# Kernel optimization log

Hardware: AMD Instinct MI355X
Metric: run time of the kernel (lower is better)

The kernel has to match this reference:

```python
import jax, jax.numpy as jnp
import numpy as np

B, S, D, H = 2, 2048, 1024, 16
DK = D // H

def setup_inputs() -> dict:
    key = jax.random.key(0)
    ks = jax.random.split(key, 9)
    def lin(k, fan_in):
        bound = 1.0 / np.sqrt(fan_in)
        kw, kb = jax.random.split(k)
        w = jax.random.uniform(kw, (D, D), jnp.float32, -bound, bound)
        b = jax.random.uniform(kb, (D,), jnp.float32, -bound, bound)
        return w, b
    Wq_w, Wq_b = lin(ks[0], D)
    Wk_w, Wk_b = lin(ks[1], D)
    Wv_w, Wv_b = lin(ks[2], D)
    Wo_w, Wo_b = lin(ks[3], D)
    x = jax.random.normal(ks[4], (B, S, D), jnp.float32)
    mask = jnp.ones((B, 1, 1, S), jnp.int32)
    return {"x": x, "mask": mask,
            "Wq_w": Wq_w, "Wq_b": Wq_b, "Wk_w": Wk_w, "Wk_b": Wk_b,
            "Wv_w": Wv_w, "Wv_b": Wv_b, "Wo_w": Wo_w, "Wo_b": Wo_b}

def reference(x, mask, Wq_w, Wq_b, Wk_w, Wk_b, Wv_w, Wv_b, Wo_w, Wo_b):
    b, s, d = x.shape
    def split_heads(t):  # [B,S,D] -> [B,H,S,DK]
        return t.reshape(b, s, H, DK).transpose(0, 2, 1, 3)
    Q = split_heads(x @ Wq_w.T + Wq_b)
    K = split_heads(x @ Wk_w.T + Wk_b)
    V = split_heads(x @ Wv_w.T + Wv_b)
    scale = 1.0 / jnp.sqrt(jnp.float32(DK))
    scores = jnp.einsum('bhqd,bhkd->bhqk', Q, K) * scale  # [B,H,S,S]
    scores = jnp.where(mask == 0, jnp.float32(-1e9), scores)
    attn = jax.nn.softmax(scores, axis=-1)
    context = jnp.einsum('bhqk,bhkd->bhqd', attn, V)  # [B,H,S,DK]
    context = context.transpose(0, 2, 1, 3).reshape(b, s, d)
    return context @ Wo_w.T + Wo_b
```

## Files before the change

kernel.cpp:

```cpp
#include <hip/hip_runtime.h>
#include <hip/hip_bf16.h>


#define DEV __device__ __forceinline__

typedef __bf16 bf16_t;
typedef __bf16 bf16x8 __attribute__((ext_vector_type(8)));
typedef float f32x4 __attribute__((ext_vector_type(4)));

constexpr int Ss = 2048, Dd = 1024, Hh = 16, DKk = 64;

DEV void gload_lds16(const void* g, void* l) {
  __builtin_amdgcn_global_load_lds(
      (__attribute__((address_space(1))) void*)(g),
      (__attribute__((address_space(3))) void*)(l), 16, 0, 0);
}

DEV bf16_t f2b(float v) { return (bf16_t)v; }

DEV void cvt16_core(const float* src, bf16_t* dst) {
  const float4* s4 = (const float4*)src;
  float4 a = s4[0], b = s4[1], c = s4[2], d = s4[3];
  bf16x8 lo = {f2b(a.x), f2b(a.y), f2b(a.z), f2b(a.w), f2b(b.x), f2b(b.y), f2b(b.z), f2b(b.w)};
  bf16x8 hi = {f2b(c.x), f2b(c.y), f2b(c.z), f2b(c.w), f2b(d.x), f2b(d.y), f2b(d.z), f2b(d.w)};
  *(bf16x8*)dst = lo;
  *(bf16x8*)(dst + 8) = hi;
}

__global__ __launch_bounds__(256) void cvt16(const float* __restrict__ x,
                                             bf16_t* __restrict__ xb) {
  size_t i = ((size_t)blockIdx.x * 256 + threadIdx.x) * 16;
  cvt16_core(x + i, xb + i);
}

__global__ __launch_bounds__(256) void cvt_w4(
    const float* __restrict__ s0, const float* __restrict__ s1,
    const float* __restrict__ s2, const float* __restrict__ s3,
    bf16_t* __restrict__ dst) {
  int z = blockIdx.y;
  const float* s = (z == 0) ? s0 : ((z == 1) ? s1 : ((z == 2) ? s2 : s3));
  size_t i = ((size_t)blockIdx.x * 256 + threadIdx.x) * 16;
  cvt16_core(s + i, dst + (size_t)z * (1u << 20) + i);
}

template <bool WB16>
__global__ __launch_bounds__(256) void gemm_qkv(
    const bf16_t* __restrict__ A,
    const float* __restrict__ W0, const float* __restrict__ W1, const float* __restrict__ W2,
    const bf16_t* __restrict__ Wb,
    const float* __restrict__ b0, const float* __restrict__ b1, const float* __restrict__ b2,
    bf16_t* __restrict__ o0, bf16_t* __restrict__ o1, bf16_t* __restrict__ o2) {
  const int z = blockIdx.z;
  const float* Wf = (z == 0) ? W0 : ((z == 1) ? W1 : W2);
  const bf16_t* Wbf = Wb + (size_t)z * (1u << 20);
  const float* bias = (z == 0) ? b0 : ((z == 1) ? b1 : b2);
  bf16_t* out = (z == 0) ? o0 : ((z == 1) ? o1 : o2);

  __shared__ __align__(16) bf16_t As[128 * 32];
  __shared__ __align__(16) bf16_t Ws[128 * 32];

  const int tid = threadIdx.x;
  const int lane = tid & 63, w = tid >> 6;
  const int quad = lane >> 4, c = lane & 15;
  const int wm = w >> 1, wn = w & 1;
  const int m0 = blockIdx.y * 128, n0 = blockIdx.x * 128;
  const int trow = tid >> 1, tcol = (tid & 1) * 16;
  const int srow = lane >> 2, scol = (lane & 3) * 8;

  const f32x4 vzero = {0.f, 0.f, 0.f, 0.f};
  f32x4 acc[4][4];
  for (int i = 0; i < 4; i++)
    for (int j = 0; j < 4; j++) acc[i][j] = vzero;

  for (int k0 = 0; k0 < 1024; k0 += 32) {
    for (int r = 0; r < 2; r++) {
      int row = r * 64 + w * 16;
      gload_lds16(&A[(size_t)(m0 + row + srow) * 1024 + k0 + scol], &As[row * 32]);
      if (WB16)
        gload_lds16(&Wbf[(size_t)(n0 + row + srow) * 1024 + k0 + scol], &Ws[row * 32]);
    }
    if (!WB16)
      cvt16_core(&Wf[(size_t)(n0 + trow) * 1024 + k0 + tcol], &Ws[trow * 32 + tcol]);
    __syncthreads();

    bf16x8 af[4], bfr[4];
    for (int i = 0; i < 4; i++)
      af[i] = *(const bf16x8*)&As[(wm * 64 + i * 16 + c) * 32 + quad * 8];
    for (int j = 0; j < 4; j++)
      bfr[j] = *(const bf16x8*)&Ws[(wn * 64 + j * 16 + c) * 32 + quad * 8];
    for (int i = 0; i < 4; i++)
      for (int j = 0; j < 4; j++)
        acc[i][j] = __builtin_amdgcn_mfma_f32_16x16x32_bf16(af[i], bfr[j], acc[i][j], 0, 0, 0);
    __syncthreads();
  }

  for (int j = 0; j < 4; j++) {
    int n = n0 + wn * 64 + j * 16 + c;
    float bv = bias[n];
    for (int i = 0; i < 4; i++) {
      int mbase = m0 + wm * 64 + i * 16 + quad * 4;
      for (int r = 0; r < 4; r++) {
        int m = mbase + r;
        float v = acc[i][j][r] + bv;
        int b_ = m >> 11, s_ = m & 2047, h_ = n >> 6, dk_ = n & 63;
        if (z < 2)
          out[((size_t)(b_ * Hh + h_) * Ss + s_) * DKk + dk_] = f2b(v);
        else
          out[((size_t)(b_ * Hh + h_) * DKk + dk_) * Ss + s_] = f2b(v);
      }
    }
  }
}

__global__ __launch_bounds__(256) void attn_fwd(
    const bf16_t* __restrict__ Q, const bf16_t* __restrict__ K,
    const bf16_t* __restrict__ Vt, const int* __restrict__ mask,
    bf16_t* __restrict__ ctx) {
  __shared__ __align__(16) bf16_t Ks[64 * 64];
  __shared__ __align__(16) bf16_t Vts[64 * 64];
  __shared__ __align__(16) bf16_t Ps[4][16 * 72];

  const int tid = threadIdx.x, lane = tid & 63, w = tid >> 6;
  const int quad = lane >> 4, c = lane & 15;
  const int bh = blockIdx.y, b_ = bh >> 4, h_ = bh & 15;
  const int q0 = blockIdx.x * 64 + w * 16;
  const size_t head = (size_t)bh * Ss * DKk;

  bf16x8 qf[2];
  for (int ks = 0; ks < 2; ks++)
    qf[ks] = *(const bf16x8*)&Q[head + (size_t)(q0 + c) * DKk + ks * 32 + quad * 8];

  const bf16_t oneb = f2b(1.0f);
  const bf16x8 ones = {oneb, oneb, oneb, oneb, oneb, oneb, oneb, oneb};

  const f32x4 vzero = {0.f, 0.f, 0.f, 0.f};
  f32x4 o[4];
  for (int j = 0; j < 4; j++) o[j] = vzero;
  f32x4 ol = vzero;

  const int sr = lane >> 3;
  const int gc = (lane & 7) ^ sr;
  const int c7 = c & 7;

  for (int kt = 0; kt < Ss / 64; kt++) {
    __syncthreads();
    for (int r = 0; r < 2; r++) {
      int row = r * 32 + w * 8;
      gload_lds16(&K[head + (size_t)(kt * 64 + row + sr) * 64 + gc * 8], &Ks[row * 64]);
      gload_lds16(&Vt[head + (size_t)(row + sr) * Ss + kt * 64 + gc * 8], &Vts[row * 64]);
    }
    __syncthreads();

    f32x4 sc[4];
    for (int ni = 0; ni < 4; ni++) sc[ni] = vzero;
    for (int ks = 0; ks < 2; ks++) {
      int pc = ((ks * 4 + quad) ^ c7) * 8;
      for (int ni = 0; ni < 4; ni++) {
        bf16x8 kf = *(const bf16x8*)&Ks[(ni * 16 + c) * 64 + pc];
        sc[ni] = __builtin_amdgcn_mfma_f32_16x16x32_bf16(qf[ks], kf, sc[ni], 0, 0, 0);
      }
    }

    for (int ni = 0; ni < 4; ni++) {
      int mk = mask[b_ * Ss + kt * 64 + ni * 16 + c];
      for (int r = 0; r < 4; r++) {
        float p = __expf(sc[ni][r] * 0.125f);
        sc[ni][r] = mk ? p : 0.f;
      }
    }

    for (int ni = 0; ni < 4; ni++)
      for (int r = 0; r < 4; r++)
        Ps[w][(quad * 4 + r) * 72 + ni * 16 + c] = f2b(sc[ni][r]);

    for (int ks = 0; ks < 2; ks++) {
      bf16x8 pf = *(const bf16x8*)&Ps[w][c * 72 + ks * 32 + quad * 8];
      int pc = ((ks * 4 + quad) ^ c7) * 8;
      for (int j = 0; j < 4; j++) {
        bf16x8 vf = *(const bf16x8*)&Vts[(j * 16 + c) * 64 + pc];
        o[j] = __builtin_amdgcn_mfma_f32_16x16x32_bf16(pf, vf, o[j], 0, 0, 0);
      }
      ol = __builtin_amdgcn_mfma_f32_16x16x32_bf16(pf, ones, ol, 0, 0, 0);
    }
  }

  float inv[4];
  for (int r = 0; r < 4; r++) inv[r] = 1.0f / ol[r];
  for (int j = 0; j < 4; j++)
    for (int r = 0; r < 4; r++) {
      int s_ = q0 + quad * 4 + r;
      ctx[((size_t)(b_ * Ss + s_)) * Dd + h_ * 64 + j * 16 + c] = f2b(o[j][r] * inv[r]);
    }
}

template <bool WB16>
__global__ __launch_bounds__(256) void gemm_out(
    const bf16_t* __restrict__ A, const float* __restrict__ Wf,
    const bf16_t* __restrict__ Wb, const float* __restrict__ bias,
    float* __restrict__ out) {
  __shared__ __align__(16) bf16_t As[128 * 32];
  __shared__ __align__(16) bf16_t Ws[128 * 32];

  const int tid = threadIdx.x;
  const int lane = tid & 63, w = tid >> 6;
  const int quad = lane >> 4, c = lane & 15;
  const int wm = w >> 1, wn = w & 1;
  const int m0 = blockIdx.y * 128, n0 = blockIdx.x * 128;
  const int trow = tid >> 1, tcol = (tid & 1) * 16;
  const int srow = lane >> 2, scol = (lane & 3) * 8;

  const f32x4 vzero = {0.f, 0.f, 0.f, 0.f};
  f32x4 acc[4][4];
  for (int i = 0; i < 4; i++)
    for (int j = 0; j < 4; j++) acc[i][j] = vzero;

  for (int k0 = 0; k0 < 1024; k0 += 32) {
    for (int r = 0; r < 2; r++) {
      int row = r * 64 + w * 16;
      gload_lds16(&A[(size_t)(m0 + row + srow) * 1024 + k0 + scol], &As[row * 32]);
      if (WB16)
        gload_lds16(&Wb[(size_t)(n0 + row + srow) * 1024 + k0 + scol], &Ws[row * 32]);
    }
    if (!WB16)
      cvt16_core(&Wf[(size_t)(n0 + trow) * 1024 + k0 + tcol], &Ws[trow * 32 + tcol]);
    __syncthreads();

    bf16x8 af[4], bfr[4];
    for (int i = 0; i < 4; i++)
      af[i] = *(const bf16x8*)&As[(wm * 64 + i * 16 + c) * 32 + quad * 8];
    for (int j = 0; j < 4; j++)
      bfr[j] = *(const bf16x8*)&Ws[(wn * 64 + j * 16 + c) * 32 + quad * 8];
    for (int i = 0; i < 4; i++)
      for (int j = 0; j < 4; j++)
        acc[i][j] = __builtin_amdgcn_mfma_f32_16x16x32_bf16(af[i], bfr[j], acc[i][j], 0, 0, 0);
    __syncthreads();
  }

  for (int j = 0; j < 4; j++) {
    int n = n0 + wn * 64 + j * 16 + c;
    float bv = bias[n];
    for (int i = 0; i < 4; i++) {
      int mbase = m0 + wm * 64 + i * 16 + quad * 4;
      for (int r = 0; r < 4; r++)
        out[(size_t)(mbase + r) * 1024 + n] = acc[i][j][r] + bv;
    }
  }
}

extern "C" void kernel_launch(void* const* d_in, const int* in_sizes, int n_in,
                              void* d_out, int out_size, void* d_ws, size_t ws_size,
                              hipStream_t stream) {
  const float* x  = (const float*)d_in[0];
  const int* mask = (const int*)d_in[1];
  const float* Wq = (const float*)d_in[2];
  const float* bq = (const float*)d_in[3];
  const float* Wk = (const float*)d_in[4];
  const float* bk = (const float*)d_in[5];
  const float* Wv = (const float*)d_in[6];
  const float* bv = (const float*)d_in[7];
  const float* Wo = (const float*)d_in[8];
  const float* bo = (const float*)d_in[9];
  float* out = (float*)d_out;

  bf16_t* ws = (bf16_t*)d_ws;
  const size_t QKV_ELEMS = (size_t)2 * Hh * Ss * DKk;
  bf16_t* xb  = ws;
  bf16_t* Qb  = ws + QKV_ELEMS;
  bf16_t* Kb  = ws + 2 * QKV_ELEMS;
  bf16_t* Vt  = ws + 3 * QKV_ELEMS;
  bf16_t* Wb  = ws + 4 * QKV_ELEMS;
  bf16_t* ctx = xb;

  const bool wb16 = ws_size >= (size_t)40 * 1024 * 1024;

  cvt16<<<dim3(1024), 256, 0, stream>>>(x, xb);
  if (wb16) {
    cvt_w4<<<dim3(256, 4), 256, 0, stream>>>(Wq, Wk, Wv, Wo, Wb);
    gemm_qkv<true><<<dim3(8, 32, 3), 256, 0, stream>>>(
        xb, Wq, Wk, Wv, Wb, bq, bk, bv, Qb, Kb, Vt);
  } else {
    gemm_qkv<false><<<dim3(8, 32, 3), 256, 0, stream>>>(
        xb, Wq, Wk, Wv, ws , bq, bk, bv, Qb, Kb, Vt);
  }
  attn_fwd<<<dim3(Ss / 64, 2 * Hh), 256, 0, stream>>>(Qb, Kb, Vt, mask, ctx);
  if (wb16)
    gemm_out<true><<<dim3(8, 32), 256, 0, stream>>>(ctx, Wo, Wb + 3 * (1u << 20), bo, out);
  else
    gemm_out<false><<<dim3(8, 32), 256, 0, stream>>>(ctx, Wo, ws , bo, out);
}
```

Baseline: 220.7 us.

## Fuse conversion kernels, double query rows per attention wave, halve out-GEMM M tile

Merges the x and weight fp32-to-bf16 conversions into one launch to drop a kernel launch. The attention kernel now gives each wave 32 query rows instead of 16, so every K/V tile loaded into LDS is reused twice as much and there are half as many blocks; the P scratch buffer gets an XOR-swizzled layout to avoid bank conflicts. The output GEMM uses 64-row M tiles, doubling its block count for better occupancy across CUs. The trade-off is more registers per attention wave and fewer attention blocks in flight.

```diff
diff --git a/kernel.cpp b/kernel.cpp
--- a/kernel.cpp
+++ b/kernel.cpp
@@ -33,14 +33,22 @@
   cvt16_core(x + i, xb + i);
 }
 
-__global__ __launch_bounds__(256) void cvt_w4(
-    const float* __restrict__ s0, const float* __restrict__ s1,
-    const float* __restrict__ s2, const float* __restrict__ s3,
-    bf16_t* __restrict__ dst) {
-  int z = blockIdx.y;
-  const float* s = (z == 0) ? s0 : ((z == 1) ? s1 : ((z == 2) ? s2 : s3));
+__global__ __launch_bounds__(256) void cvt_all(
+    const float* __restrict__ x,
+    const float* __restrict__ wq, const float* __restrict__ wk,
+    const float* __restrict__ wv, const float* __restrict__ wo,
+    bf16_t* __restrict__ xb, bf16_t* __restrict__ Wb) {
   size_t i = ((size_t)blockIdx.x * 256 + threadIdx.x) * 16;
-  cvt16_core(s + i, dst + (size_t)z * (1u << 20) + i);
+  const size_t XN = (size_t)4 << 20;
+  if (i < XN) {
+    cvt16_core(x + i, xb + i);
+  } else {
+    size_t j = i - XN;
+    int z = (int)(j >> 20);
+    size_t o = j & (((size_t)1 << 20) - 1);
+    const float* s = (z == 0) ? wq : ((z == 1) ? wk : ((z == 2) ? wv : wo));
+    cvt16_core(s + o, Wb + j);
+  }
 }
 
 template <bool WB16>
@@ -118,29 +126,31 @@
     bf16_t* __restrict__ ctx) {
   __shared__ __align__(16) bf16_t Ks[64 * 64];
   __shared__ __align__(16) bf16_t Vts[64 * 64];
-  __shared__ __align__(16) bf16_t Ps[4][16 * 72];
+  __shared__ __align__(16) bf16_t Ps[4][32 * 64];
 
   const int tid = threadIdx.x, lane = tid & 63, w = tid >> 6;
   const int quad = lane >> 4, c = lane & 15;
+  const int c7 = c & 7;
   const int bh = blockIdx.y, b_ = bh >> 4, h_ = bh & 15;
-  const int q0 = blockIdx.x * 64 + w * 16;
+  const int q0 = blockIdx.x * 128 + w * 32;
   const size_t head = (size_t)bh * Ss * DKk;
 
-  bf16x8 qf[2];
-  for (int ks = 0; ks < 2; ks++)
-    qf[ks] = *(const bf16x8*)&Q[head + (size_t)(q0 + c) * DKk + ks * 32 + quad * 8];
+  bf16x8 qf[2][2];
+  for (int mi = 0; mi < 2; mi++)
+    for (int ks = 0; ks < 2; ks++)
+      qf[mi][ks] = *(const bf16x8*)&Q[head + (size_t)(q0 + mi * 16 + c) * DKk + ks * 32 + quad * 8];
 
   const bf16_t oneb = f2b(1.0f);
   const bf16x8 ones = {oneb, oneb, oneb, oneb, oneb, oneb, oneb, oneb};
 
   const f32x4 vzero = {0.f, 0.f, 0.f, 0.f};
-  f32x4 o[4];
-  for (int j = 0; j < 4; j++) o[j] = vzero;
-  f32x4 ol = vzero;
+  f32x4 o[2][4];
+  for (int mi = 0; mi < 2; mi++)
+    for (int j = 0; j < 4; j++) o[mi][j] = vzero;
+  f32x4 ol[2] = {vzero, vzero};
 
   const int sr = lane >> 3;
   const int gc = (lane & 7) ^ sr;
-  const int c7 = c & 7;
 
   for (int kt = 0; kt < Ss / 64; kt++) {
     __syncthreads();
@@ -151,46 +161,59 @@
     }
     __syncthreads();
 
-    f32x4 sc[4];
-    for (int ni = 0; ni < 4; ni++) sc[ni] = vzero;
+    f32x4 sc[2][4];
+    for (int mi = 0; mi < 2; mi++)
+      for (int ni = 0; ni < 4; ni++) sc[mi][ni] = vzero;
     for (int ks = 0; ks < 2; ks++) {
       int pc = ((ks * 4 + quad) ^ c7) * 8;
       for (int ni = 0; ni < 4; ni++) {
         bf16x8 kf = *(const bf16x8*)&Ks[(ni * 16 + c) * 64 + pc];
-        sc[ni] = __builtin_amdgcn_mfma_f32_16x16x32_bf16(qf[ks], kf, sc[ni], 0, 0, 0);
+        sc[0][ni] = __builtin_amdgcn_mfma_f32_16x16x32_bf16(qf[0][ks], kf, sc[0][ni], 0, 0, 0);
+        sc[1][ni] = __builtin_amdgcn_mfma_f32_16x16x32_bf16(qf[1][ks], kf, sc[1][ni], 0, 0, 0);
       }
     }
 
     for (int ni = 0; ni < 4; ni++) {
       int mk = mask[b_ * Ss + kt * 64 + ni * 16 + c];
-      for (int r = 0; r < 4; r++) {
-        float p = __expf(sc[ni][r] * 0.125f);
-        sc[ni][r] = mk ? p : 0.f;
-      }
-    }
-
-    for (int ni = 0; ni < 4; ni++)
-      for (int r = 0; r < 4; r++)
-        Ps[w][(quad * 4 + r) * 72 + ni * 16 + c] = f2b(sc[ni][r]);
+      for (int mi = 0; mi < 2; mi++)
+        for (int r = 0; r < 4; r++) {
+          float p = __expf(sc[mi][ni][r] * 0.125f);
+          sc[mi][ni][r] = mk ? p : 0.f;
+        }
+    }
+
+    for (int mi = 0; mi < 2; mi++)
+      for (int ni = 0; ni < 4; ni++)
+        for (int r = 0; r < 4; r++) {
+          int ql = mi * 16 + quad * 4 + r;
+          int chunk = (ni * 2 + (c >> 3)) ^ (ql & 7);
+          Ps[w][ql * 64 + chunk * 8 + c7] = f2b(sc[mi][ni][r]);
+        }
 
     for (int ks = 0; ks < 2; ks++) {
-      bf16x8 pf = *(const bf16x8*)&Ps[w][c * 72 + ks * 32 + quad * 8];
       int pc = ((ks * 4 + quad) ^ c7) * 8;
+      bf16x8 pf0 = *(const bf16x8*)&Ps[w][(c)*64 + pc];
+      bf16x8 pf1 = *(const bf16x8*)&Ps[w][(16 + c) * 64 + pc];
       for (int j = 0; j < 4; j++) {
         bf16x8 vf = *(const bf16x8*)&Vts[(j * 16 + c) * 64 + pc];
-        o[j] = __builtin_amdgcn_mfma_f32_16x16x32_bf16(pf, vf, o[j], 0, 0, 0);
-      }
-      ol = __builtin_amdgcn_mfma_f32_16x16x32_bf16(pf, ones, ol, 0, 0, 0);
-    }
-  }
-
-  float inv[4];
-  for (int r = 0; r < 4; r++) inv[r] = 1.0f / ol[r];
-  for (int j = 0; j < 4; j++)
-    for (int r = 0; r < 4; r++) {
-      int s_ = q0 + quad * 4 + r;
-      ctx[((size_t)(b_ * Ss + s_)) * Dd + h_ * 64 + j * 16 + c] = f2b(o[j][r] * inv[r]);
-    }
+        o[0][j] = __builtin_amdgcn_mfma_f32_16x16x32_bf16(pf0, vf, o[0][j], 0, 0, 0);
+        o[1][j] = __builtin_amdgcn_mfma_f32_16x16x32_bf16(pf1, vf, o[1][j], 0, 0, 0);
+      }
+      ol[0] = __builtin_amdgcn_mfma_f32_16x16x32_bf16(pf0, ones, ol[0], 0, 0, 0);
+      ol[1] = __builtin_amdgcn_mfma_f32_16x16x32_bf16(pf1, ones, ol[1], 0, 0, 0);
+    }
+  }
+
+  for (int mi = 0; mi < 2; mi++) {
+    float inv[4];
+    for (int r = 0; r < 4; r++) inv[r] = 1.0f / ol[mi][r];
+    for (int j = 0; j < 4; j++)
+      for (int r = 0; r < 4; r++) {
+        int s_ = q0 + mi * 16 + quad * 4 + r;
+        ctx[((size_t)(b_ * Ss + s_)) * Dd + h_ * 64 + j * 16 + c] =
+            f2b(o[mi][j][r] * inv[r]);
+      }
+  }
 }
 
 template <bool WB16>
@@ -198,39 +221,40 @@
     const bf16_t* __restrict__ A, const float* __restrict__ Wf,
     const bf16_t* __restrict__ Wb, const float* __restrict__ bias,
     float* __restrict__ out) {
-  __shared__ __align__(16) bf16_t As[128 * 32];
+  __shared__ __align__(16) bf16_t As[64 * 32];
   __shared__ __align__(16) bf16_t Ws[128 * 32];
 
   const int tid = threadIdx.x;
   const int lane = tid & 63, w = tid >> 6;
   const int quad = lane >> 4, c = lane & 15;
   const int wm = w >> 1, wn = w & 1;
-  const int m0 = blockIdx.y * 128, n0 = blockIdx.x * 128;
+  const int m0 = blockIdx.y * 64, n0 = blockIdx.x * 128;
   const int trow = tid >> 1, tcol = (tid & 1) * 16;
   const int srow = lane >> 2, scol = (lane & 3) * 8;
 
   const f32x4 vzero = {0.f, 0.f, 0.f, 0.f};
-  f32x4 acc[4][4];
-  for (int i = 0; i < 4; i++)
+  f32x4 acc[2][4];
+  for (int i = 0; i < 2; i++)
     for (int j = 0; j < 4; j++) acc[i][j] = vzero;
 
   for (int k0 = 0; k0 < 1024; k0 += 32) {
-    for (int r = 0; r < 2; r++) {
-      int row = r * 64 + w * 16;
-      gload_lds16(&A[(size_t)(m0 + row + srow) * 1024 + k0 + scol], &As[row * 32]);
-      if (WB16)
+    gload_lds16(&A[(size_t)(m0 + w * 16 + srow) * 1024 + k0 + scol], &As[(w * 16) * 32]);
+    if (WB16) {
+      for (int r = 0; r < 2; r++) {
+        int row = r * 64 + w * 16;
         gload_lds16(&Wb[(size_t)(n0 + row + srow) * 1024 + k0 + scol], &Ws[row * 32]);
-    }
-    if (!WB16)
+      }
+    } else {
       cvt16_core(&Wf[(size_t)(n0 + trow) * 1024 + k0 + tcol], &Ws[trow * 32 + tcol]);
-    __syncthreads();
-
-    bf16x8 af[4], bfr[4];
-    for (int i = 0; i < 4; i++)
-      af[i] = *(const bf16x8*)&As[(wm * 64 + i * 16 + c) * 32 + quad * 8];
+    }
+    __syncthreads();
+
+    bf16x8 af[2], bfr[4];
+    for (int i = 0; i < 2; i++)
+      af[i] = *(const bf16x8*)&As[(wm * 32 + i * 16 + c) * 32 + quad * 8];
     for (int j = 0; j < 4; j++)
       bfr[j] = *(const bf16x8*)&Ws[(wn * 64 + j * 16 + c) * 32 + quad * 8];
-    for (int i = 0; i < 4; i++)
+    for (int i = 0; i < 2; i++)
       for (int j = 0; j < 4; j++)
         acc[i][j] = __builtin_amdgcn_mfma_f32_16x16x32_bf16(af[i], bfr[j], acc[i][j], 0, 0, 0);
     __syncthreads();
@@ -239,8 +263,8 @@
   for (int j = 0; j < 4; j++) {
     int n = n0 + wn * 64 + j * 16 + c;
     float bv = bias[n];
-    for (int i = 0; i < 4; i++) {
-      int mbase = m0 + wm * 64 + i * 16 + quad * 4;
+    for (int i = 0; i < 2; i++) {
+      int mbase = m0 + wm * 32 + i * 16 + quad * 4;
       for (int r = 0; r < 4; r++)
         out[(size_t)(mbase + r) * 1024 + n] = acc[i][j][r] + bv;
     }
@@ -273,18 +297,18 @@
 
   const bool wb16 = ws_size >= (size_t)40 * 1024 * 1024;
 
-  cvt16<<<dim3(1024), 256, 0, stream>>>(x, xb);
   if (wb16) {
-    cvt_w4<<<dim3(256, 4), 256, 0, stream>>>(Wq, Wk, Wv, Wo, Wb);
+    cvt_all<<<dim3(2048), 256, 0, stream>>>(x, Wq, Wk, Wv, Wo, xb, Wb);
     gemm_qkv<true><<<dim3(8, 32, 3), 256, 0, stream>>>(
         xb, Wq, Wk, Wv, Wb, bq, bk, bv, Qb, Kb, Vt);
   } else {
+    cvt16<<<dim3(1024), 256, 0, stream>>>(x, xb);
     gemm_qkv<false><<<dim3(8, 32, 3), 256, 0, stream>>>(
         xb, Wq, Wk, Wv, ws , bq, bk, bv, Qb, Kb, Vt);
   }
-  attn_fwd<<<dim3(Ss / 64, 2 * Hh), 256, 0, stream>>>(Qb, Kb, Vt, mask, ctx);
+  attn_fwd<<<dim3(Ss / 128, 2 * Hh), 256, 0, stream>>>(Qb, Kb, Vt, mask, ctx);
   if (wb16)
-    gemm_out<true><<<dim3(8, 32), 256, 0, stream>>>(ctx, Wo, Wb + 3 * (1u << 20), bo, out);
+    gemm_out<true><<<dim3(8, 64), 256, 0, stream>>>(ctx, Wo, Wb + 3 * (1u << 20), bo, out);
   else
-    gemm_out<false><<<dim3(8, 32), 256, 0, stream>>>(ctx, Wo, ws , bo, out);
-}
+    gemm_out<false><<<dim3(8, 64), 256, 0, stream>>>(ctx, Wo, ws , bo, out);
+}
```

New measurement: 220.4 us. Within noise of the previous version (-0.1%).
